# Performance work log

Hardware: AMD Instinct MI355X
Metric: run time of the kernel (lower is better)

## Reference

```python
import jax, jax.numpy as jnp
import numpy as np

B, N, D = 4096, 32768, 256


def setup_inputs() -> dict:
    key = jax.random.key(0)
    kx, kp = jax.random.split(key)
    x = jax.random.normal(kx, (B, D), dtype=jnp.float32)
    prototypes = jax.random.normal(kp, (N, D), dtype=jnp.float32)
    return {"x": x, "prototypes": prototypes}


def reference(x, prototypes):
    # Brute-force L2 1-NN: faiss IndexFlatL2 exact search, k=1, then gather
    x_sq = jnp.sum(x * x, axis=-1, keepdims=True)            # [B, 1]
    p_sq = jnp.sum(prototypes * prototypes, axis=-1)          # [N]
    dists = x_sq + p_sq[None, :] - 2.0 * (x @ prototypes.T)   # [B, N]
    idx = jnp.argmin(dists, axis=-1)                          # [B]
    return prototypes[idx]                                    # [B, D]
```

## Files before the change

### kernel.cpp

```cpp
#include <hip/hip_runtime.h>
#include <stdint.h>


#define NB 4096
#define NP 32768
#define ND 256
#define NG 512
#define MARGIN 2.0f

typedef __attribute__((ext_vector_type(8))) __bf16 bf16x8;
typedef __attribute__((ext_vector_type(4))) __bf16 bf16x4;
typedef __attribute__((ext_vector_type(4))) float f32x4;

static constexpr size_t OFF_PSQ = 0;
static constexpr size_t OFF_XB  = 131072;
static constexpr size_t OFF_PB  = OFF_XB + (size_t)NB * ND * 2;
static constexpr size_t OFF_BM  = OFF_PB + (size_t)NP * ND * 2;
static constexpr size_t WS_NEED = OFF_BM + (size_t)NB * NG * 4;

__device__ __forceinline__ void gload_lds16(const void* g, void* l) {
    __builtin_amdgcn_global_load_lds(
        (const __attribute__((address_space(1))) uint32_t*)g,
        (__attribute__((address_space(3))) uint32_t*)l, 16, 0, 0);
}
__device__ __forceinline__ unsigned fkey(float f) {
    unsigned u = __float_as_uint(f);
    return (u & 0x80000000u) ? ~u : (u | 0x80000000u);
}
__device__ __forceinline__ float fkey_inv(unsigned u) {
    unsigned o = (u & 0x80000000u) ? (u & 0x7FFFFFFFu) : ~u;
    return __uint_as_float(o);
}
__device__ __forceinline__ unsigned long long umin64(unsigned long long a,
                                                     unsigned long long b) {
    return a < b ? a : b;
}
__device__ __forceinline__ unsigned umin32(unsigned a, unsigned b) {
    return a < b ? a : b;
}

__global__ void prep_kernel(const float* __restrict__ X, const float* __restrict__ P,
                            float* __restrict__ psq, __bf16* __restrict__ Xb,
                            __bf16* __restrict__ Pb) {
    int row  = blockIdx.x * 4 + (threadIdx.x >> 6);
    int lane = threadIdx.x & 63;
    if (row < NP) {
        f32x4 v = ((const f32x4*)(P + (size_t)row * ND))[lane];
        bf16x4 b;
        b.x = (__bf16)v.x; b.y = (__bf16)v.y; b.z = (__bf16)v.z; b.w = (__bf16)v.w;
        ((bf16x4*)(Pb + (size_t)row * ND))[lane] = b;
        float s = v.x*v.x + v.y*v.y + v.z*v.z + v.w*v.w;
        #pragma unroll
        for (int off = 32; off > 0; off >>= 1) s += __shfl_down(s, off);
        if (lane == 0) psq[row] = s;
    } else {
        int r = row - NP;
        f32x4 v = ((const f32x4*)(X + (size_t)r * ND))[lane];
        bf16x4 b;
        b.x = (__bf16)v.x; b.y = (__bf16)v.y; b.z = (__bf16)v.z; b.w = (__bf16)v.w;
        ((bf16x4*)(Xb + (size_t)r * ND))[lane] = b;
    }
}

__device__ __forceinline__ void stage_tile(const __bf16* __restrict__ Xb,
                                           const __bf16* __restrict__ Pb,
                                           char* As, char* Bs,
                                           int bm, int bn, int k0, int tid) {
    const int wbase = tid & ~63;
    #pragma unroll
    for (int i = 0; i < 4; ++i) {
        const int c  = i * 512 + tid;
        const int fm = c >> 7;
        const int ks = (c >> 6) & 1;
        const int kg = (c >> 4) & 3;
        const int fr = c & 15;
        const int kk = k0 + ks * 32 + kg * 8;
        gload_lds16(Xb + (size_t)(bm + fm * 16 + fr) * ND + kk,
                    As + (size_t)(i * 512 + wbase) * 16);
        gload_lds16(Pb + (size_t)(bn + fm * 16 + fr) * ND + kk,
                    Bs + (size_t)(i * 512 + wbase) * 16);
    }
}

__device__ __forceinline__ void compute_step(const char* As, const char* Bs,
                                             int wm, int wn, int lane,
                                             f32x4 acc[8][4]) {
    #pragma unroll
    for (int ks = 0; ks < 2; ++ks) {
        bf16x8 a[8], b[4];
        #pragma unroll
        for (int mi = 0; mi < 8; ++mi)
            a[mi] = *(const bf16x8*)(As +
                     (size_t)(((wm * 8 + mi) * 2 + ks) * 64 + lane) * 16);
        #pragma unroll
        for (int ni = 0; ni < 4; ++ni)
            b[ni] = *(const bf16x8*)(Bs +
                     (size_t)(((wn * 4 + ni) * 2 + ks) * 64 + lane) * 16);
        #pragma unroll
        for (int mi = 0; mi < 8; ++mi)
            #pragma unroll
            for (int ni = 0; ni < 4; ++ni)
                acc[mi][ni] = __builtin_amdgcn_mfma_f32_16x16x32_bf16(
                    a[mi], b[ni], acc[mi][ni], 0, 0, 0);
    }
}

__global__ __launch_bounds__(512, 2)
void nn_bf16_kernel(const __bf16* __restrict__ Xb, const __bf16* __restrict__ Pb,
                    const float* __restrict__ psq, unsigned* __restrict__ blockmin) {
    __shared__ __align__(16) char smem[131072];
    char* As0 = smem;
    char* Bs0 = smem + 32768;
    char* As1 = smem + 65536;
    char* Bs1 = smem + 98304;

    const int tid  = threadIdx.x;
    const int lane = tid & 63;
    const int wave = tid >> 6;
    const int wm = wave >> 2, wn = wave & 3;
    const int bm = blockIdx.x * 256;
    const int bn = blockIdx.y * 256;

    f32x4 acc[8][4];
    #pragma unroll
    for (int i = 0; i < 8; ++i)
        #pragma unroll
        for (int j = 0; j < 4; ++j) acc[i][j] = (f32x4){0.f, 0.f, 0.f, 0.f};

    stage_tile(Xb, Pb, As0, Bs0, bm, bn, 0, tid);
    __syncthreads();
    stage_tile(Xb, Pb, As1, Bs1, bm, bn, 64, tid);
    compute_step(As0, Bs0, wm, wn, lane, acc);
    __syncthreads();
    stage_tile(Xb, Pb, As0, Bs0, bm, bn, 128, tid);
    compute_step(As1, Bs1, wm, wn, lane, acc);
    __syncthreads();
    stage_tile(Xb, Pb, As1, Bs1, bm, bn, 192, tid);
    compute_step(As0, Bs0, wm, wn, lane, acc);
    __syncthreads();
    compute_step(As1, Bs1, wm, wn, lane, acc);

    const int cl = lane & 15;
    const int rg = lane >> 4;
    float cq[4];
    #pragma unroll
    for (int ni = 0; ni < 4; ++ni) cq[ni] = psq[bn + wn * 64 + ni * 16 + cl];
    const int gidx = blockIdx.y * 4 + wn;
    #pragma unroll
    for (int mi = 0; mi < 8; ++mi) {
        #pragma unroll
        for (int r = 0; r < 4; ++r) {
            int row = bm + wm * 128 + mi * 16 + rg * 4 + r;
            float best = fmaf(-2.f, acc[mi][0][r], cq[0]);
            #pragma unroll
            for (int ni = 1; ni < 4; ++ni)
                best = fminf(best, fmaf(-2.f, acc[mi][ni][r], cq[ni]));
            #pragma unroll
            for (int m = 1; m < 16; m <<= 1)
                best = fminf(best, __shfl_xor(best, m));
            if (cl == 0) blockmin[(size_t)row * NG + gidx] = fkey(best);
        }
    }
}

__global__ __launch_bounds__(256)
void rescore_kernel(const float* __restrict__ X, const float* __restrict__ P,
                    const float* __restrict__ psq,
                    const unsigned* __restrict__ blockmin,
                    float* __restrict__ out) {
    __shared__ float Xs[256];
    __shared__ float part[256];
    __shared__ unsigned keymin[256];
    __shared__ unsigned short cand[NG];
    __shared__ int cnt;
    __shared__ unsigned bcol_s;

    const int row = blockIdx.x;
    const int tid = threadIdx.x;
    const unsigned* bmr = blockmin + (size_t)row * NG;

    unsigned k0 = bmr[tid], k1 = bmr[tid + 256];
    if (tid < 64)
        ((f32x4*)Xs)[tid] = ((const f32x4*)(X + (size_t)row * ND))[tid];
    if (tid == 0) cnt = 0;
    keymin[tid] = umin32(k0, k1);
    __syncthreads();
    #pragma unroll
    for (int s = 128; s > 0; s >>= 1) {
        if (tid < s) keymin[tid] = umin32(keymin[tid], keymin[tid + s]);
        __syncthreads();
    }
    unsigned thr = fkey(fkey_inv(keymin[0]) + MARGIN);
    if (k0 <= thr) cand[atomicAdd(&cnt, 1)] = (unsigned short)tid;
    if (k1 <= thr) cand[atomicAdd(&cnt, 1)] = (unsigned short)(tid + 256);
    __syncthreads();

    const int n     = cnt;
    const int ct    = tid & 63;
    const int cpart = tid >> 6;
    unsigned long long best = 0xFFFFFFFFFFFFFFFFull;
    for (int c = 0; c < n; ++c) {
        int g = cand[c];
        int col = g * 64 + ct;
        const f32x4* p4 = (const f32x4*)(P + (size_t)col * ND + cpart * 64);
        const f32x4* x4 = (const f32x4*)(Xs + cpart * 64);
        float s = 0.f;
        #pragma unroll
        for (int i = 0; i < 16; ++i) {
            f32x4 pv = p4[i], xv = x4[i];
            s = fmaf(xv.x, pv.x, s); s = fmaf(xv.y, pv.y, s);
            s = fmaf(xv.z, pv.z, s); s = fmaf(xv.w, pv.w, s);
        }
        part[tid] = s;
        __syncthreads();
        if (tid < 64) {
            int col2 = g * 64 + tid;
            float tot = part[tid] + part[tid + 64] + part[tid + 128] + part[tid + 192];
            float d = fmaf(-2.f, tot, psq[col2]);
            best = umin64(best, ((unsigned long long)fkey(d) << 32) |
                                (unsigned long long)col2);
        }
        __syncthreads();
    }
    if (tid < 64) {
        #pragma unroll
        for (int m = 1; m < 64; m <<= 1)
            best = umin64(best, __shfl_xor(best, m));
        if (tid == 0) bcol_s = (unsigned)(best & 0xFFFFFFFFull);
    }
    __syncthreads();
    unsigned bc = bcol_s;
    if (tid < 64)
        ((f32x4*)(out + (size_t)row * ND))[tid] =
            ((const f32x4*)(P + (size_t)bc * ND))[tid];
}

#define BM1 128
#define BN1 128
#define BK1 32
#define LDA1 132

__global__ void psq_init_kernel(const float* __restrict__ P, float* __restrict__ psq,
                                unsigned long long* __restrict__ minpack) {
    int row  = blockIdx.x * 4 + (threadIdx.x >> 6);
    int lane = threadIdx.x & 63;
    float4 p4 = ((const float4*)(P + (size_t)row * ND))[lane];
    float s = p4.x*p4.x + p4.y*p4.y + p4.z*p4.z + p4.w*p4.w;
    #pragma unroll
    for (int off = 32; off > 0; off >>= 1) s += __shfl_down(s, off);
    if (lane == 0) psq[row] = s;
    int gid = blockIdx.x * blockDim.x + threadIdx.x;
    if (gid < NB) minpack[gid] = 0xFFFFFFFFFFFFFFFFull;
}

__global__ __launch_bounds__(256, 2)
void nn_main_kernel(const float* __restrict__ X, const float* __restrict__ P,
                    const float* __restrict__ psq,
                    unsigned long long* __restrict__ minpack) {
    __shared__ __align__(16) char smem_raw[2 * BK1 * LDA1 * 4];
    float (*As)[LDA1] = (float (*)[LDA1])smem_raw;
    float (*Bs)[LDA1] = (float (*)[LDA1])(smem_raw + BK1 * LDA1 * 4);
    const int bm  = blockIdx.y * BM1;
    const int bn  = blockIdx.x * BN1;
    const int tid = threadIdx.x;
    const int tx  = tid & 15;
    const int ty  = tid >> 4;
    float acc[8][8];
    #pragma unroll
    for (int i = 0; i < 8; ++i)
        #pragma unroll
        for (int j = 0; j < 8; ++j) acc[i][j] = 0.f;
    const int lrow = tid >> 3;
    const int lk   = (tid & 7) * 4;
    for (int k0 = 0; k0 < ND; k0 += BK1) {
        #pragma unroll
        for (int p = 0; p < 4; ++p) {
            int r = p * 32 + lrow;
            float4 a = *(const float4*)(X + (size_t)(bm + r) * ND + k0 + lk);
            As[lk+0][r] = a.x; As[lk+1][r] = a.y; As[lk+2][r] = a.z; As[lk+3][r] = a.w;
            float4 b = *(const float4*)(P + (size_t)(bn + r) * ND + k0 + lk);
            Bs[lk+0][r] = b.x; Bs[lk+1][r] = b.y; Bs[lk+2][r] = b.z; Bs[lk+3][r] = b.w;
        }
        __syncthreads();
        #pragma unroll 4
        for (int k = 0; k < BK1; ++k) {
            float4 a0 = *(const float4*)&As[k][ty*8];
            float4 a1 = *(const float4*)&As[k][ty*8 + 4];
            float4 b0 = *(const float4*)&Bs[k][tx*4];
            float4 b1 = *(const float4*)&Bs[k][64 + tx*4];
            float av[8] = {a0.x,a0.y,a0.z,a0.w,a1.x,a1.y,a1.z,a1.w};
            float bv[8] = {b0.x,b0.y,b0.z,b0.w,b1.x,b1.y,b1.z,b1.w};
            #pragma unroll
            for (int i = 0; i < 8; ++i)
                #pragma unroll
                for (int j = 0; j < 8; ++j)
                    acc[i][j] = fmaf(av[i], bv[j], acc[i][j]);
        }
        __syncthreads();
    }
    unsigned long long (*red)[16] = (unsigned long long (*)[16])smem_raw;
    float cj[8];
    int   jglob[8];
    #pragma unroll
    for (int j = 0; j < 8; ++j) {
        int c = (j < 4) ? (tx*4 + j) : (64 + tx*4 + (j - 4));
        jglob[j] = bn + c;
        cj[j]    = psq[bn + c];
    }
    #pragma unroll
    for (int i = 0; i < 8; ++i) {
        float best = 0.f; unsigned bidx = 0u; bool first = true;
        #pragma unroll
        for (int j = 0; j < 8; ++j) {
            float s = fmaf(-2.f, acc[i][j], cj[j]);
            if (first || s < best) { best = s; bidx = (unsigned)jglob[j]; first = false; }
        }
        unsigned u = fkey(best);
        red[ty*8 + i][tx] = ((unsigned long long)u << 32) | (unsigned long long)bidx;
    }
    __syncthreads();
    if (tid < BM1) {
        unsigned long long m = red[tid][0];
        #pragma unroll
        for (int t = 1; t < 16; ++t) m = umin64(m, red[tid][t]);
        atomicMin(&minpack[bm + tid], m);
    }
}

__global__ void gather_kernel(const float* __restrict__ P,
                              const unsigned long long* __restrict__ minpack,
                              float* __restrict__ out) {
    int row = blockIdx.x;
    unsigned idx = (unsigned)(minpack[row] & 0xFFFFFFFFull);
    int lane = threadIdx.x;
    ((float4*)(out + (size_t)row * ND))[lane] =
        ((const float4*)(P + (size_t)idx * ND))[lane];
}

extern "C" void kernel_launch(void* const* d_in, const int* in_sizes, int n_in,
                              void* d_out, int out_size, void* d_ws, size_t ws_size,
                              hipStream_t stream) {
    const float* X = (const float*)d_in[0];
    const float* P = (const float*)d_in[1];
    float* out = (float*)d_out;
    char* w = (char*)d_ws;

    if (ws_size >= WS_NEED) {
        float* psq = (float*)(w + OFF_PSQ);
        __bf16* Xb = (__bf16*)(w + OFF_XB);
        __bf16* Pb = (__bf16*)(w + OFF_PB);
        unsigned* blockmin = (unsigned*)(w + OFF_BM);

        prep_kernel<<<(NP + NB) / 4, 256, 0, stream>>>(X, P, psq, Xb, Pb);
        dim3 grid(NB / 256, NP / 256);
        nn_bf16_kernel<<<grid, dim3(512), 0, stream>>>(Xb, Pb, psq, blockmin);
        rescore_kernel<<<NB, 256, 0, stream>>>(X, P, psq, blockmin, out);
    } else {
        float* psq = (float*)w;
        unsigned long long* minpack = (unsigned long long*)(w + (size_t)NP * 4);
        psq_init_kernel<<<NP / 4, 256, 0, stream>>>(P, psq, minpack);
        dim3 grid(NP / BN1, NB / BM1);
        nn_main_kernel<<<grid, dim3(256), 0, stream>>>(X, P, psq, minpack);
        gather_kernel<<<NB, 64, 0, stream>>>(P, minpack, out);
    }
}
```

Before: 210.8 us.

## Restructure bf16 GEMM into persistent sweep with register-resident X tiles

Replaces the 256x256 output-tile grid with 256 blocks that each hold a 128-row X tile in registers for the full K and sweep a 4096-column slice of prototypes. Prototype tiles stream through double-buffered LDS with explicit vmcnt waits and barriers, and the per-group row minimum is written out after each 256-column tile. This removes the repeated staging of X and the per-tile launch and prologue cost, at the price of heavy register use (32 bf16x8 A fragments) and a smaller grid that may underfill the GPU.

```diff
diff --git a/kernel.cpp b/kernel.cpp
--- a/kernel.cpp
+++ b/kernel.cpp
@@ -7,6 +7,11 @@
 #define ND 256
 #define NG 512
 #define MARGIN 2.0f
+
+#define NSPLIT 8
+#define CPB    4096
+#define NCT    16
+#define NITER  32
 
 typedef __attribute__((ext_vector_type(8))) __bf16 bf16x8;
 typedef __attribute__((ext_vector_type(4))) __bf16 bf16x4;
@@ -62,103 +67,120 @@
     }
 }
 
-__device__ __forceinline__ void stage_tile(const __bf16* __restrict__ Xb,
-                                           const __bf16* __restrict__ Pb,
-                                           char* As, char* Bs,
-                                           int bm, int bn, int k0, int tid) {
-    const int wbase = tid & ~63;
-    #pragma unroll
-    for (int i = 0; i < 4; ++i) {
-        const int c  = i * 512 + tid;
-        const int fm = c >> 7;
-        const int ks = (c >> 6) & 1;
-        const int kg = (c >> 4) & 3;
-        const int fr = c & 15;
-        const int kk = k0 + ks * 32 + kg * 8;
-        gload_lds16(Xb + (size_t)(bm + fm * 16 + fr) * ND + kk,
-                    As + (size_t)(i * 512 + wbase) * 16);
-        gload_lds16(Pb + (size_t)(bn + fm * 16 + fr) * ND + kk,
-                    Bs + (size_t)(i * 512 + wbase) * 16);
-    }
-}
-
-__device__ __forceinline__ void compute_step(const char* As, const char* Bs,
-                                             int wm, int wn, int lane,
-                                             f32x4 acc[8][4]) {
-    #pragma unroll
-    for (int ks = 0; ks < 2; ++ks) {
-        bf16x8 a[8], b[4];
-        #pragma unroll
-        for (int mi = 0; mi < 8; ++mi)
-            a[mi] = *(const bf16x8*)(As +
-                     (size_t)(((wm * 8 + mi) * 2 + ks) * 64 + lane) * 16);
-        #pragma unroll
-        for (int ni = 0; ni < 4; ++ni)
-            b[ni] = *(const bf16x8*)(Bs +
-                     (size_t)(((wn * 4 + ni) * 2 + ks) * 64 + lane) * 16);
-        #pragma unroll
-        for (int mi = 0; mi < 8; ++mi)
-            #pragma unroll
-            for (int ni = 0; ni < 4; ++ni)
-                acc[mi][ni] = __builtin_amdgcn_mfma_f32_16x16x32_bf16(
-                    a[mi], b[ni], acc[mi][ni], 0, 0, 0);
-    }
-}
-
 __global__ __launch_bounds__(512, 2)
-void nn_bf16_kernel(const __bf16* __restrict__ Xb, const __bf16* __restrict__ Pb,
-                    const float* __restrict__ psq, unsigned* __restrict__ blockmin) {
-    __shared__ __align__(16) char smem[131072];
-    char* As0 = smem;
-    char* Bs0 = smem + 32768;
-    char* As1 = smem + 65536;
-    char* Bs1 = smem + 98304;
+void nn_sweep_kernel(const __bf16* __restrict__ Xb, const __bf16* __restrict__ Pb,
+                     const float* __restrict__ psq, unsigned* __restrict__ blockmin) {
+    __shared__ __align__(16) char Bs[2][65536];
 
     const int tid  = threadIdx.x;
     const int lane = tid & 63;
     const int wave = tid >> 6;
     const int wm = wave >> 2, wn = wave & 3;
-    const int bm = blockIdx.x * 256;
-    const int bn = blockIdx.y * 256;
-
-    f32x4 acc[8][4];
-    #pragma unroll
-    for (int i = 0; i < 8; ++i)
+    const int bid    = blockIdx.x;
+    const int mblk   = bid >> 3;
+    const int nsplit = bid & 7;
+    const int bm     = mblk * 128;
+    const int nbase0 = nsplit * CPB;
+    const int fr = lane & 15, kg = lane >> 4;
+
+    bf16x8 a[4][8];
+    #pragma unroll
+    for (int mi = 0; mi < 4; ++mi)
+        #pragma unroll
+        for (int ks = 0; ks < 8; ++ks)
+            a[mi][ks] = *(const bf16x8*)(Xb +
+                (size_t)(bm + wm * 64 + mi * 16 + fr) * ND + ks * 32 + kg * 8);
+    __builtin_amdgcn_sched_barrier(0);
+
+    f32x4 acc[4][4];
+    #pragma unroll
+    for (int i = 0; i < 4; ++i)
         #pragma unroll
         for (int j = 0; j < 4; ++j) acc[i][j] = (f32x4){0.f, 0.f, 0.f, 0.f};
 
-    stage_tile(Xb, Pb, As0, Bs0, bm, bn, 0, tid);
-    __syncthreads();
-    stage_tile(Xb, Pb, As1, Bs1, bm, bn, 64, tid);
-    compute_step(As0, Bs0, wm, wn, lane, acc);
-    __syncthreads();
-    stage_tile(Xb, Pb, As0, Bs0, bm, bn, 128, tid);
-    compute_step(As1, Bs1, wm, wn, lane, acc);
-    __syncthreads();
-    stage_tile(Xb, Pb, As1, Bs1, bm, bn, 192, tid);
-    compute_step(As0, Bs0, wm, wn, lane, acc);
-    __syncthreads();
-    compute_step(As1, Bs1, wm, wn, lane, acc);
-
-    const int cl = lane & 15;
-    const int rg = lane >> 4;
-    float cq[4];
-    #pragma unroll
-    for (int ni = 0; ni < 4; ++ni) cq[ni] = psq[bn + wn * 64 + ni * 16 + cl];
-    const int gidx = blockIdx.y * 4 + wn;
-    #pragma unroll
-    for (int mi = 0; mi < 8; ++mi) {
-        #pragma unroll
-        for (int r = 0; r < 4; ++r) {
-            int row = bm + wm * 128 + mi * 16 + rg * 4 + r;
-            float best = fmaf(-2.f, acc[mi][0][r], cq[0]);
+    const int wbase = tid & ~63;
+
+    auto stage = [&](int ct, int kh, char* buf) {
+        const int nbase = nbase0 + ct * 256;
+        #pragma unroll
+        for (int i = 0; i < 8; ++i) {
+            const int c   = i * 512 + tid;
+            const int fn  = c >> 8;
+            const int ks  = (c >> 6) & 3;
+            const int l   = c & 63;
+            const int lkg = l >> 4, lfr = l & 15;
+            gload_lds16(Pb + (size_t)(nbase + fn * 16 + lfr) * ND +
+                            (kh * 4 + ks) * 32 + lkg * 8,
+                        buf + (size_t)(i * 512 + wbase) * 16);
+        }
+    };
+
+    stage(0, 0, (char*)Bs[0]);
+    __builtin_amdgcn_sched_barrier(0);
+    stage(0, 1, (char*)Bs[1]);
+    __builtin_amdgcn_sched_barrier(0);
+
+    for (int ct = 0; ct < NCT; ++ct) {
+        #pragma unroll
+        for (int kh = 0; kh < 2; ++kh) {
+            const int t = ct * 2 + kh;
+            if (t < NITER - 1) asm volatile("s_waitcnt vmcnt(8)" ::: "memory");
+            else               asm volatile("s_waitcnt vmcnt(0)" ::: "memory");
+            __builtin_amdgcn_sched_barrier(0);
+            __builtin_amdgcn_s_barrier();
+            __builtin_amdgcn_sched_barrier(0);
+
+            const char* buf = (const char*)Bs[t & 1];
             #pragma unroll
-            for (int ni = 1; ni < 4; ++ni)
-                best = fminf(best, fmaf(-2.f, acc[mi][ni][r], cq[ni]));
-            #pragma unroll
-            for (int m = 1; m < 16; m <<= 1)
-                best = fminf(best, __shfl_xor(best, m));
-            if (cl == 0) blockmin[(size_t)row * NG + gidx] = fkey(best);
+            for (int ks = 0; ks < 4; ++ks) {
+                bf16x8 b[4];
+                #pragma unroll
+                for (int ni = 0; ni < 4; ++ni)
+                    b[ni] = *(const bf16x8*)(buf +
+                        (size_t)((((wn * 4 + ni) * 4 + ks) * 64 + lane)) * 16);
+                #pragma unroll
+                for (int mi = 0; mi < 4; ++mi)
+                    #pragma unroll
+                    for (int ni = 0; ni < 4; ++ni)
+                        acc[mi][ni] = __builtin_amdgcn_mfma_f32_16x16x32_bf16(
+                            a[mi][kh * 4 + ks], b[ni], acc[mi][ni], 0, 0, 0);
+            }
+
+            if (kh == 1) {
+                const int colb = nbase0 + ct * 256 + wn * 64;
+                float cq[4];
+                #pragma unroll
+                for (int ni = 0; ni < 4; ++ni) cq[ni] = psq[colb + ni * 16 + fr];
+                const int g = nsplit * 64 + ct * 4 + wn;
+                #pragma unroll
+                for (int mi = 0; mi < 4; ++mi) {
+                    #pragma unroll
+                    for (int r = 0; r < 4; ++r) {
+                        float d = fmaf(-2.f, acc[mi][0][r], cq[0]);
+                        #pragma unroll
+                        for (int ni = 1; ni < 4; ++ni)
+                            d = fminf(d, fmaf(-2.f, acc[mi][ni][r], cq[ni]));
+                        #pragma unroll
+                        for (int m = 1; m < 16; m <<= 1)
+                            d = fminf(d, __shfl_xor(d, m));
+                        if (fr == 0)
+                            blockmin[(size_t)(bm + wm * 64 + mi * 16 + kg * 4 + r)
+                                     * NG + g] = fkey(d);
+                    }
+                }
+                #pragma unroll
+                for (int i = 0; i < 4; ++i)
+                    #pragma unroll
+                    for (int j = 0; j < 4; ++j)
+                        acc[i][j] = (f32x4){0.f, 0.f, 0.f, 0.f};
+            }
+
+            asm volatile("s_waitcnt lgkmcnt(0)" ::: "memory");
+            __builtin_amdgcn_sched_barrier(0);
+            __builtin_amdgcn_s_barrier();
+            __builtin_amdgcn_sched_barrier(0);
+            const int t2 = t + 2;
+            if (t2 < NITER) stage(t2 >> 1, t2 & 1, (char*)Bs[t & 1]);
         }
     }
 }
@@ -352,8 +374,8 @@
         unsigned* blockmin = (unsigned*)(w + OFF_BM);
 
         prep_kernel<<<(NP + NB) / 4, 256, 0, stream>>>(X, P, psq, Xb, Pb);
-        dim3 grid(NB / 256, NP / 256);
-        nn_bf16_kernel<<<grid, dim3(512), 0, stream>>>(Xb, Pb, psq, blockmin);
+        nn_sweep_kernel<<<(NB / 128) * NSPLIT, 512, 0, stream>>>(Xb, Pb, psq,
+                                                                 blockmin);
         rescore_kernel<<<NB, 256, 0, stream>>>(X, P, psq, blockmin, out);
     } else {
         float* psq = (float*)w;
```

Result: slower. 271.2 us (+28.6%).

## Split GEMM main loop into finer phases with interleaved loads and barriers

Applied to the files above, without the earlier changes.

The bf16 distance GEMM main loop is restructured into four phases per K tile. Each phase issues a half-tile global-to-LDS load for the next buffer, waits on explicit vmcnt counters, and runs a 4x4 MFMA sub-block at raised wave priority. The aim is to replace the coarse stage/compute/syncthreads double-buffer with finer-grained overlap of memory and MFMA work. In exchange it relies on hand-tuned vmcnt values and raw s_barrier without an LDS wait, and it adds more barriers per tile.

```diff
diff --git a/kernel.cpp b/kernel.cpp
--- a/kernel.cpp
+++ b/kernel.cpp
@@ -17,6 +17,8 @@
 static constexpr size_t OFF_PB  = OFF_XB + (size_t)NB * ND * 2;
 static constexpr size_t OFF_BM  = OFF_PB + (size_t)NP * ND * 2;
 static constexpr size_t WS_NEED = OFF_BM + (size_t)NB * NG * 4;
+
+#define VMCNT(n) asm volatile("s_waitcnt vmcnt(" #n ")" ::: "memory")
 
 __device__ __forceinline__ void gload_lds16(const void* g, void* l) {
     __builtin_amdgcn_global_load_lds(
@@ -62,57 +64,10 @@
     }
 }
 
-__device__ __forceinline__ void stage_tile(const __bf16* __restrict__ Xb,
-                                           const __bf16* __restrict__ Pb,
-                                           char* As, char* Bs,
-                                           int bm, int bn, int k0, int tid) {
-    const int wbase = tid & ~63;
-    #pragma unroll
-    for (int i = 0; i < 4; ++i) {
-        const int c  = i * 512 + tid;
-        const int fm = c >> 7;
-        const int ks = (c >> 6) & 1;
-        const int kg = (c >> 4) & 3;
-        const int fr = c & 15;
-        const int kk = k0 + ks * 32 + kg * 8;
-        gload_lds16(Xb + (size_t)(bm + fm * 16 + fr) * ND + kk,
-                    As + (size_t)(i * 512 + wbase) * 16);
-        gload_lds16(Pb + (size_t)(bn + fm * 16 + fr) * ND + kk,
-                    Bs + (size_t)(i * 512 + wbase) * 16);
-    }
-}
-
-__device__ __forceinline__ void compute_step(const char* As, const char* Bs,
-                                             int wm, int wn, int lane,
-                                             f32x4 acc[8][4]) {
-    #pragma unroll
-    for (int ks = 0; ks < 2; ++ks) {
-        bf16x8 a[8], b[4];
-        #pragma unroll
-        for (int mi = 0; mi < 8; ++mi)
-            a[mi] = *(const bf16x8*)(As +
-                     (size_t)(((wm * 8 + mi) * 2 + ks) * 64 + lane) * 16);
-        #pragma unroll
-        for (int ni = 0; ni < 4; ++ni)
-            b[ni] = *(const bf16x8*)(Bs +
-                     (size_t)(((wn * 4 + ni) * 2 + ks) * 64 + lane) * 16);
-        #pragma unroll
-        for (int mi = 0; mi < 8; ++mi)
-            #pragma unroll
-            for (int ni = 0; ni < 4; ++ni)
-                acc[mi][ni] = __builtin_amdgcn_mfma_f32_16x16x32_bf16(
-                    a[mi], b[ni], acc[mi][ni], 0, 0, 0);
-    }
-}
-
 __global__ __launch_bounds__(512, 2)
-void nn_bf16_kernel(const __bf16* __restrict__ Xb, const __bf16* __restrict__ Pb,
-                    const float* __restrict__ psq, unsigned* __restrict__ blockmin) {
+void nn_8ph_kernel(const __bf16* __restrict__ Xb, const __bf16* __restrict__ Pb,
+                   const float* __restrict__ psq, unsigned* __restrict__ blockmin) {
     __shared__ __align__(16) char smem[131072];
-    char* As0 = smem;
-    char* Bs0 = smem + 32768;
-    char* As1 = smem + 65536;
-    char* Bs1 = smem + 98304;
 
     const int tid  = threadIdx.x;
     const int lane = tid & 63;
@@ -127,18 +82,119 @@
         #pragma unroll
         for (int j = 0; j < 4; ++j) acc[i][j] = (f32x4){0.f, 0.f, 0.f, 0.f};
 
-    stage_tile(Xb, Pb, As0, Bs0, bm, bn, 0, tid);
-    __syncthreads();
-    stage_tile(Xb, Pb, As1, Bs1, bm, bn, 64, tid);
-    compute_step(As0, Bs0, wm, wn, lane, acc);
-    __syncthreads();
-    stage_tile(Xb, Pb, As0, Bs0, bm, bn, 128, tid);
-    compute_step(As1, Bs1, wm, wn, lane, acc);
-    __syncthreads();
-    stage_tile(Xb, Pb, As1, Bs1, bm, bn, 192, tid);
-    compute_step(As0, Bs0, wm, wn, lane, acc);
-    __syncthreads();
-    compute_step(As1, Bs1, wm, wn, lane, acc);
+    const int wbase16 = (tid & ~63) * 16;
+
+    auto stageA = [&](int buf, int ks, int t) {
+        char* dst = smem + (size_t)(buf * 2 + ks) * 16384;
+        #pragma unroll
+        for (int i = 0; i < 2; ++i) {
+            const int c  = i * 512 + tid;
+            const int fm = c >> 6;
+            const int l  = c & 63;
+            gload_lds16(Xb + (size_t)(bm + fm * 16 + (l & 15)) * ND +
+                            t * 64 + ks * 32 + (l >> 4) * 8,
+                        dst + i * 512 * 16 + wbase16);
+        }
+    };
+    auto stageB = [&](int buf, int ks, int t) {
+        char* dst = smem + 65536 + (size_t)(buf * 2 + ks) * 16384;
+        #pragma unroll
+        for (int i = 0; i < 2; ++i) {
+            const int c  = i * 512 + tid;
+            const int fn = c >> 6;
+            const int l  = c & 63;
+            gload_lds16(Pb + (size_t)(bn + fn * 16 + (l & 15)) * ND +
+                            t * 64 + ks * 32 + (l >> 4) * 8,
+                        dst + i * 512 * 16 + wbase16);
+        }
+    };
+
+    stageA(0, 0, 0); stageB(0, 0, 0); stageA(0, 1, 0); stageB(0, 1, 0);
+
+    #pragma unroll
+    for (int t = 0; t < 4; ++t) {
+        const int b  = t & 1;
+        const int nb = b ^ 1;
+        const char* Ap0 = smem + (size_t)(b * 2 + 0) * 16384;
+        const char* Ap1 = smem + (size_t)(b * 2 + 1) * 16384;
+        const char* Bp0 = smem + 65536 + (size_t)(b * 2 + 0) * 16384;
+        const char* Bp1 = smem + 65536 + (size_t)(b * 2 + 1) * 16384;
+
+        if (t < 3) stageA(nb, 0, t + 1);
+        if (t < 3) { VMCNT(6); } else { VMCNT(4); }
+        __builtin_amdgcn_s_barrier();
+        __builtin_amdgcn_sched_barrier(0);
+        bf16x8 b0[4], a0[4];
+        #pragma unroll
+        for (int ni = 0; ni < 4; ++ni)
+            b0[ni] = *(const bf16x8*)(Bp0 +
+                      (size_t)((wn * 4 + ni) * 64 + lane) * 16);
+        #pragma unroll
+        for (int mi = 0; mi < 4; ++mi)
+            a0[mi] = *(const bf16x8*)(Ap0 +
+                      (size_t)((wm * 8 + mi) * 64 + lane) * 16);
+        __builtin_amdgcn_s_setprio(1);
+        #pragma unroll
+        for (int mi = 0; mi < 4; ++mi)
+            #pragma unroll
+            for (int ni = 0; ni < 4; ++ni)
+                acc[mi][ni] = __builtin_amdgcn_mfma_f32_16x16x32_bf16(
+                    a0[mi], b0[ni], acc[mi][ni], 0, 0, 0);
+        __builtin_amdgcn_s_setprio(0);
+
+        if (t < 3) stageB(nb, 0, t + 1);
+        __builtin_amdgcn_s_barrier();
+        __builtin_amdgcn_sched_barrier(0);
+        #pragma unroll
+        for (int mi = 0; mi < 4; ++mi)
+            a0[mi] = *(const bf16x8*)(Ap0 +
+                      (size_t)((wm * 8 + 4 + mi) * 64 + lane) * 16);
+        __builtin_amdgcn_s_setprio(1);
+        #pragma unroll
+        for (int mi = 0; mi < 4; ++mi)
+            #pragma unroll
+            for (int ni = 0; ni < 4; ++ni)
+                acc[4 + mi][ni] = __builtin_amdgcn_mfma_f32_16x16x32_bf16(
+                    a0[mi], b0[ni], acc[4 + mi][ni], 0, 0, 0);
+        __builtin_amdgcn_s_setprio(0);
+
+        if (t < 3) stageA(nb, 1, t + 1);
+        if (t < 3) { VMCNT(6); } else { VMCNT(0); }
+        __builtin_amdgcn_s_barrier();
+        __builtin_amdgcn_sched_barrier(0);
+        #pragma unroll
+        for (int ni = 0; ni < 4; ++ni)
+            b0[ni] = *(const bf16x8*)(Bp1 +
+                      (size_t)((wn * 4 + ni) * 64 + lane) * 16);
+        #pragma unroll
+        for (int mi = 0; mi < 4; ++mi)
+            a0[mi] = *(const bf16x8*)(Ap1 +
+                      (size_t)((wm * 8 + mi) * 64 + lane) * 16);
+        __builtin_amdgcn_s_setprio(1);
+        #pragma unroll
+        for (int mi = 0; mi < 4; ++mi)
+            #pragma unroll
+            for (int ni = 0; ni < 4; ++ni)
+                acc[mi][ni] = __builtin_amdgcn_mfma_f32_16x16x32_bf16(
+                    a0[mi], b0[ni], acc[mi][ni], 0, 0, 0);
+        __builtin_amdgcn_s_setprio(0);
+
+        if (t < 3) stageB(nb, 1, t + 1);
+        __builtin_amdgcn_s_barrier();
+        __builtin_amdgcn_sched_barrier(0);
+        #pragma unroll
+        for (int mi = 0; mi < 4; ++mi)
+            a0[mi] = *(const bf16x8*)(Ap1 +
+                      (size_t)((wm * 8 + 4 + mi) * 64 + lane) * 16);
+        __builtin_amdgcn_s_setprio(1);
+        #pragma unroll
+        for (int mi = 0; mi < 4; ++mi)
+            #pragma unroll
+            for (int ni = 0; ni < 4; ++ni)
+                acc[4 + mi][ni] = __builtin_amdgcn_mfma_f32_16x16x32_bf16(
+                    a0[mi], b0[ni], acc[4 + mi][ni], 0, 0, 0);
+        __builtin_amdgcn_s_setprio(0);
+    }
 
     const int cl = lane & 15;
     const int rg = lane >> 4;
@@ -353,7 +409,7 @@
 
         prep_kernel<<<(NP + NB) / 4, 256, 0, stream>>>(X, P, psq, Xb, Pb);
         dim3 grid(NB / 256, NP / 256);
-        nn_bf16_kernel<<<grid, dim3(512), 0, stream>>>(Xb, Pb, psq, blockmin);
+        nn_8ph_kernel<<<grid, dim3(512), 0, stream>>>(Xb, Pb, psq, blockmin);
         rescore_kernel<<<NB, 256, 0, stream>>>(X, P, psq, blockmin, out);
     } else {
         float* psq = (float*)w;
```

Result: faster. 198.5 us (-5.9%).
